# Kernel optimization log

Measured on AMD Instinct MI355X. Metric: run time of the kernel, lower is better.

## Reference

```python
import jax, jax.numpy as jnp
import numpy as np
import math

B, T, D, H, L, V = 2, 1024, 768, 12, 4, 50257
HD = D // H
ROPE_PCT = 0.5
MAX_WL = 10000.0
EPS = 1e-5


def setup_inputs() -> dict:
    key = jax.random.key(0)
    ks = jax.random.split(key, 8)
    s = 0.02
    return {
        "idx": jax.random.randint(ks[0], (B, T), 0, V, dtype=jnp.int32),
        "wte": jax.random.normal(ks[1], (V, D), jnp.float32) * s,
        "ln1_g": jnp.ones((L, D), jnp.float32),
        "ln1_b": jnp.zeros((L, D), jnp.float32),
        "Wqkv": jax.random.normal(ks[2], (L, D, 3 * D), jnp.float32) * s,
        "bqkv": jnp.zeros((L, 3 * D), jnp.float32),
        "Wo": jax.random.normal(ks[3], (L, D, D), jnp.float32) * s,
        "bo": jnp.zeros((L, D), jnp.float32),
        "ln2_g": jnp.ones((L, D), jnp.float32),
        "ln2_b": jnp.zeros((L, D), jnp.float32),
        "Wfc": jax.random.normal(ks[4], (L, D, 4 * D), jnp.float32) * s,
        "bfc": jnp.zeros((L, 4 * D), jnp.float32),
        "Wp": jax.random.normal(ks[5], (L, 4 * D, D), jnp.float32) * s,
        "bp": jnp.zeros((L, D), jnp.float32),
        "lnf_g": jnp.ones((D,), jnp.float32),
        "lnf_b": jnp.zeros((D,), jnp.float32),
        "Wlm": jax.random.normal(ks[6], (D, V), jnp.float32) * s,
    }


def _ln(x, g, b):
    m = x.mean(-1, keepdims=True)
    v = x.var(-1, keepdims=True)
    return (x - m) / jnp.sqrt(v + EPS) * g + b


def _gelu(x):
    return 0.5 * x * (1.0 + jnp.tanh(math.sqrt(2.0 / math.pi) * (x + 0.044715 * x ** 3)))


def _p_rope(x, positions):
    # x: [B, H, T, HD]; partial RoPE: rotate first ROPE_PCT of angle pairs, leave rest.
    rope_angles = int(ROPE_PCT * HD // 2)
    nope_angles = HD // 2 - rope_angles
    fraction = 2.0 * jnp.arange(0, rope_angles) / HD
    timescale = jnp.power(MAX_WL, fraction)
    timescale = jnp.pad(timescale, (0, nope_angles), constant_values=jnp.inf)
    sinusoid = positions[:, None] / timescale[None, :]  # [T, HD//2]; pos/inf = 0 -> no rotation
    sin, cos = jnp.sin(sinusoid), jnp.cos(sinusoid)
    first, second = jnp.split(x, 2, axis=-1)
    out = jnp.concatenate([first * cos - second * sin, second * cos + first * sin], axis=-1)
    return out.astype(x.dtype)


def reference(idx, wte, ln1_g, ln1_b, Wqkv, bqkv, Wo, bo, ln2_g, ln2_b, Wfc, bfc, Wp, bp, lnf_g, lnf_b, Wlm):
    x = wte[idx]  # [B, T, D]
    positions = jnp.arange(T, dtype=x.dtype)
    causal = jnp.tril(jnp.ones((T, T), dtype=bool))
    scale = jnp.sqrt(jnp.float32(HD)).astype(x.dtype)
    for l in range(L):
        h1 = _ln(x, ln1_g[l], ln1_b[l])
        h2 = _ln(x, ln2_g[l], ln2_b[l])  # note: both LNs read the same x (as in source)
        # attention
        qkv = h1 @ Wqkv[l] + bqkv[l]
        q, k, v = jnp.split(qkv, 3, axis=-1)
        sh = lambda t: t.reshape(B, T, H, HD).transpose(0, 2, 1, 3)
        q, k, v = sh(q), sh(k), sh(v)
        q = _p_rope(q, positions)
        k = _p_rope(k, positions)
        att = jnp.einsum('bhqd,bhkd->bhqk', q, k) / scale
        att = jnp.where(causal, att, jnp.finfo(att.dtype).min)
        att = jax.nn.softmax(att, axis=-1)
        y = jnp.einsum('bhqk,bhkd->bhqd', att, v)
        y = y.transpose(0, 2, 1, 3).reshape(B, T, D)
        x = x + (y @ Wo[l] + bo[l])
        # MLP
        h = _gelu(h2 @ Wfc[l] + bfc[l])
        x = x + (h @ Wp[l] + bp[l])
    x = _ln(x, lnf_g, lnf_b)
    logits = x @ Wlm  # [B, T, V]
    return logits
```

## Files before the change

kernel.cpp:

```cpp
#include <hip/hip_runtime.h>

typedef unsigned short u16;
typedef unsigned int u32;
typedef __attribute__((ext_vector_type(8))) short bf16x8;
typedef __attribute__((ext_vector_type(4))) float f32x4;

#define SEQ 1024
#define DM 768
#define NH 12
#define HD2 64
#define NLAYER 4
#define NVOCAB 50257
#define BT 2048

__device__ __forceinline__ u16 f2bf(float f) {
  union { float f; u32 u; } v; v.f = f;
  u32 r = v.u + 0x7FFFu + ((v.u >> 16) & 1u);
  return (u16)(r >> 16);
}
__device__ __forceinline__ float bf2f(u16 u) {
  union { u32 u; float f; } v; v.u = ((u32)u) << 16;
  return v.f;
}

__device__ __forceinline__ void glds16(const u16* g, u16* l) {
  __builtin_amdgcn_global_load_lds(
      (const __attribute__((address_space(1))) u32*)(const void*)g,
      (__attribute__((address_space(3))) u32*)(void*)l, 16, 0, 0);
}

__global__ void k_embed(const int* __restrict__ idx, const float* __restrict__ wte,
                        float* __restrict__ xf) {
  int r = blockIdx.x;
  int tok = idx[r];
  const float* s = wte + (size_t)tok * DM;
  float* d = xf + (size_t)r * DM;
  for (int c = threadIdx.x; c < DM; c += 256) d[c] = s[c];
}

__global__ void k_cvtT(const float* __restrict__ in, u16* __restrict__ out,
                       int R, int C) {
  __shared__ u16 t[32][34];
  int c0 = blockIdx.x * 32, r0 = blockIdx.y * 32;
  int tx = threadIdx.x & 31, ty = threadIdx.x >> 5;
#pragma unroll
  for (int i = 0; i < 4; ++i) {
    int r = r0 + ty + i * 8, c = c0 + tx;
    float v = (c < C) ? in[(size_t)r * C + c] : 0.f;
    t[ty + i * 8][tx] = f2bf(v);
  }
  __syncthreads();
  int cy = threadIdx.x >> 4;
  int rx = (threadIdx.x & 15) * 2;
#pragma unroll
  for (int i = 0; i < 2; ++i) {
    int c = c0 + cy + i * 16;
    if (c < C) {
      u32 wv = (u32)t[rx][cy + i * 16] | ((u32)t[rx + 1][cy + i * 16] << 16);
      *(u32*)&out[(size_t)c * R + r0 + rx] = wv;
    }
  }
}

__device__ __forceinline__ float bsum(float v, float* red) {
#pragma unroll
  for (int o = 32; o > 0; o >>= 1) v += __shfl_down(v, o);
  if ((threadIdx.x & 63) == 0) red[threadIdx.x >> 6] = v;
  __syncthreads();
  if (threadIdx.x == 0) red[4] = red[0] + red[1] + red[2] + red[3];
  __syncthreads();
  return red[4];
}

__global__ void k_ln(const float* __restrict__ x, const float* __restrict__ g1,
                     const float* __restrict__ b1, const float* __restrict__ g2,
                     const float* __restrict__ b2, u16* __restrict__ o1,
                     u16* __restrict__ o2) {
  __shared__ float red[8];
  int r = blockIdx.x;
  int t = threadIdx.x;
  const float* xr = x + (size_t)r * DM;
  float v0 = xr[t], v1 = xr[t + 256], v2 = xr[t + 512];
  float mean = bsum(v0 + v1 + v2, red) * (1.f / DM);
  float d0 = v0 - mean, d1 = v1 - mean, d2 = v2 - mean;
  float var = bsum(d0 * d0 + d1 * d1 + d2 * d2, red) * (1.f / DM);
  float rstd = rsqrtf(var + 1e-5f);
  u16* p1 = o1 + (size_t)r * DM;
  p1[t]       = f2bf(d0 * rstd * g1[t]       + b1[t]);
  p1[t + 256] = f2bf(d1 * rstd * g1[t + 256] + b1[t + 256]);
  p1[t + 512] = f2bf(d2 * rstd * g1[t + 512] + b1[t + 512]);
  if (o2) {
    u16* p2 = o2 + (size_t)r * DM;
    p2[t]       = f2bf(d0 * rstd * g2[t]       + b2[t]);
    p2[t + 256] = f2bf(d1 * rstd * g2[t + 256] + b2[t + 256]);
    p2[t + 512] = f2bf(d2 * rstd * g2[t + 512] + b2[t + 512]);
  }
}

__global__ void k_rope(const u16* __restrict__ qkvb, u16* __restrict__ qr,
                       u16* __restrict__ kr) {
  int gid = blockIdx.x * 256 + threadIdx.x;
  int j = gid & 31;
  int h = (gid >> 5) % NH;
  int t = (gid / (32 * NH)) & (SEQ - 1);
  int b = gid / (32 * NH * SEQ);
  float c = 1.f, s = 0.f;
  if (j < 16) {
    float inv = powf(10000.f, -(float)j * (1.f / 32.f));
    float ang = (float)t * inv;
    c = cosf(ang);
    s = sinf(ang);
  }
  size_t base = (size_t)(b * SEQ + t) * (3 * DM);
  size_t ob = ((size_t)(b * NH + h) * SEQ + t) * HD2 + j;
  {
    float a0 = bf2f(qkvb[base + h * HD2 + j]);
    float a1 = bf2f(qkvb[base + h * HD2 + j + 32]);
    qr[ob] = f2bf(a0 * c - a1 * s);
    qr[ob + 32] = f2bf(a1 * c + a0 * s);
  }
  {
    float a0 = bf2f(qkvb[base + DM + h * HD2 + j]);
    float a1 = bf2f(qkvb[base + DM + h * HD2 + j + 32]);
    kr[ob] = f2bf(a0 * c - a1 * s);
    kr[ob + 32] = f2bf(a1 * c + a0 * s);
  }
}

__global__ void k_vtrans(const u16* __restrict__ qkvb, u16* __restrict__ vT) {
  __shared__ u16 tile[64][65];
  int t0 = blockIdx.x * 64;
  int bh = blockIdx.y;
  int b = bh / NH, h = bh % NH;
  int rr = threadIdx.x >> 2, seg = threadIdx.x & 3;
  const u16* src = qkvb + (size_t)(b * SEQ + t0 + rr) * (3 * DM) + 2 * DM + h * HD2;
#pragma unroll
  for (int i = 0; i < 16; ++i) tile[rr][seg * 16 + i] = src[seg * 16 + i];
  __syncthreads();
  u16* dst = vT + ((size_t)bh * HD2 + rr) * SEQ + t0;
#pragma unroll
  for (int i = 0; i < 16; ++i) dst[seg * 16 + i] = tile[seg * 16 + i][rr];
}

__global__ void k_attn(const u16* __restrict__ qr, const u16* __restrict__ kr,
                       const u16* __restrict__ vT, u16* __restrict__ yb) {
  int ti = (int)gridDim.x - 1 - (int)blockIdx.x;
  int bh = blockIdx.y;
  __shared__ u16 Ps[64 * 72];
  __shared__ u16 Ks[2][4096];
  __shared__ u16 Vs[2][4096];
  int tid = threadIdx.x;
  int rr = tid >> 2, cc = tid & 3;
  int w = tid >> 6, l = tid & 63;
  int rl = l & 15, g = l >> 4;
  {
    const u16* gq = qr + ((size_t)bh * SEQ + ti * 64 + rr) * HD2;
    *(uint4*)&Ps[rr * 72 + cc * 8]      = *(const uint4*)(gq + cc * 8);
    *(uint4*)&Ps[rr * 72 + cc * 8 + 32] = *(const uint4*)(gq + cc * 8 + 32);
  }
  int srow = w * 8 + (l >> 3);
  int gs = (l & 7) ^ (l >> 3);
  const u16* gkb = kr + (size_t)bh * SEQ * HD2;
  const u16* gvb = vT + (size_t)bh * HD2 * SEQ;
  glds16(gkb + (size_t)(0 * 64 + srow) * 64 + gs * 8,      &Ks[0][w * 512]);
  glds16(gkb + (size_t)(0 * 64 + 32 + srow) * 64 + gs * 8, &Ks[0][2048 + w * 512]);
  glds16(gvb + (size_t)srow * SEQ + 0 * 64 + gs * 8,       &Vs[0][w * 512]);
  glds16(gvb + (size_t)(32 + srow) * SEQ + 0 * 64 + gs * 8,&Vs[0][2048 + w * 512]);
  __syncthreads();
  bf16x8 aq0 = *(const bf16x8*)&Ps[(w * 16 + rl) * 72 + g * 8];
  bf16x8 aq1 = *(const bf16x8*)&Ps[(w * 16 + rl) * 72 + 32 + g * 8];
  float m[4], lsum[4];
  f32x4 oacc[4] = {};
#pragma unroll
  for (int r2 = 0; r2 < 4; ++r2) { m[r2] = -3.0e38f; lsum[r2] = 0.f; }
  int qloc = w * 16 + g * 4;
  int sw = rl & 7;
  int cur = 0;
  for (int kt = 0; kt <= ti; ++kt) {
    if (kt < ti) {
      int nx = cur ^ 1;
      glds16(gkb + (size_t)((kt + 1) * 64 + srow) * 64 + gs * 8,      &Ks[nx][w * 512]);
      glds16(gkb + (size_t)((kt + 1) * 64 + 32 + srow) * 64 + gs * 8, &Ks[nx][2048 + w * 512]);
      glds16(gvb + (size_t)srow * SEQ + (kt + 1) * 64 + gs * 8,       &Vs[nx][w * 512]);
      glds16(gvb + (size_t)(32 + srow) * SEQ + (kt + 1) * 64 + gs * 8,&Vs[nx][2048 + w * 512]);
    }
    f32x4 s[4] = {};
    __builtin_amdgcn_s_setprio(1);
#pragma unroll
    for (int nt = 0; nt < 4; ++nt) {
      int r = (nt * 16 + rl) * 64;
      bf16x8 b0 = *(const bf16x8*)&Ks[cur][r + ((0 + g) ^ sw) * 8];
      bf16x8 b1 = *(const bf16x8*)&Ks[cur][r + ((4 + g) ^ sw) * 8];
      s[nt] = __builtin_amdgcn_mfma_f32_16x16x32_bf16(aq0, b0, s[nt], 0, 0, 0);
      s[nt] = __builtin_amdgcn_mfma_f32_16x16x32_bf16(aq1, b1, s[nt], 0, 0, 0);
    }
    __builtin_amdgcn_s_setprio(0);
#pragma unroll
    for (int nt = 0; nt < 4; ++nt) s[nt] *= 0.125f;
    if (kt == ti) {
#pragma unroll
      for (int nt = 0; nt < 4; ++nt) {
        int col = nt * 16 + rl;
#pragma unroll
        for (int r2 = 0; r2 < 4; ++r2)
          if (col > qloc + r2) s[nt][r2] = -3.0e38f;
      }
    }
#pragma unroll
    for (int r2 = 0; r2 < 4; ++r2) {
      float pm = fmaxf(fmaxf(s[0][r2], s[1][r2]), fmaxf(s[2][r2], s[3][r2]));
#pragma unroll
      for (int o = 1; o < 16; o <<= 1) pm = fmaxf(pm, __shfl_xor(pm, o));
      float mn = fmaxf(m[r2], pm);
      float corr = __expf(m[r2] - mn);
      float p0 = __expf(s[0][r2] - mn);
      float p1 = __expf(s[1][r2] - mn);
      float p2 = __expf(s[2][r2] - mn);
      float p3 = __expf(s[3][r2] - mn);
      float ps = p0 + p1 + p2 + p3;
#pragma unroll
      for (int o = 1; o < 16; o <<= 1) ps += __shfl_xor(ps, o);
      lsum[r2] = lsum[r2] * corr + ps;
      m[r2] = mn;
      oacc[0][r2] *= corr; oacc[1][r2] *= corr;
      oacc[2][r2] *= corr; oacc[3][r2] *= corr;
      int prow = (qloc + r2) * 72;
      Ps[prow + rl]      = f2bf(p0);
      Ps[prow + 16 + rl] = f2bf(p1);
      Ps[prow + 32 + rl] = f2bf(p2);
      Ps[prow + 48 + rl] = f2bf(p3);
    }
    bf16x8 pa0 = *(const bf16x8*)&Ps[(w * 16 + rl) * 72 + g * 8];
    bf16x8 pa1 = *(const bf16x8*)&Ps[(w * 16 + rl) * 72 + 32 + g * 8];
    __builtin_amdgcn_s_setprio(1);
#pragma unroll
    for (int nt = 0; nt < 4; ++nt) {
      int r = (nt * 16 + rl) * 64;
      bf16x8 b0 = *(const bf16x8*)&Vs[cur][r + ((0 + g) ^ sw) * 8];
      bf16x8 b1 = *(const bf16x8*)&Vs[cur][r + ((4 + g) ^ sw) * 8];
      oacc[nt] = __builtin_amdgcn_mfma_f32_16x16x32_bf16(pa0, b0, oacc[nt], 0, 0, 0);
      oacc[nt] = __builtin_amdgcn_mfma_f32_16x16x32_bf16(pa1, b1, oacc[nt], 0, 0, 0);
    }
    __builtin_amdgcn_s_setprio(0);
    __syncthreads();
    cur ^= 1;
  }
  int b = bh / NH, h = bh % NH;
  float invl[4];
#pragma unroll
  for (int r2 = 0; r2 < 4; ++r2) invl[r2] = 1.f / lsum[r2];
#pragma unroll
  for (int nt = 0; nt < 4; ++nt) {
    int d = nt * 16 + rl;
#pragma unroll
    for (int r2 = 0; r2 < 4; ++r2) {
      int trow = ti * 64 + qloc + r2;
      yb[((size_t)(b * SEQ + trow)) * DM + h * HD2 + d] = f2bf(oacc[nt][r2] * invl[r2]);
    }
  }
}

__global__ void k_logits(const u16* __restrict__ A, const u16* __restrict__ Bt,
                         float* __restrict__ outf, int M, int N, int K, int MT) {
  __shared__ u16 SM[16384];
  float* cw = (float*)SM;
  int nwg = gridDim.x;
  int id = blockIdx.x;
  if ((nwg & 7) == 0) id = (id & 7) * (nwg >> 3) + (id >> 3);
  int mt = id % MT, nt = id / MT;
  int m0 = mt * 128, n0 = nt * 128;
  int tid = threadIdx.x;
  int w = tid >> 6, l = tid & 63;
  int srow = w * 16 + (l >> 2);
  int gs = (l & 3) ^ ((l >> 3) & 3);
  const u16* gA0 = A + (size_t)(m0 + srow) * K + gs * 8;
  const u16* gA1 = A + (size_t)(m0 + 64 + srow) * K + gs * 8;
  int rb0 = n0 + srow;      if (rb0 > N - 1) rb0 = N - 1;
  int rb1 = n0 + 64 + srow; if (rb1 > N - 1) rb1 = N - 1;
  const u16* gB0 = Bt + (size_t)rb0 * K + gs * 8;
  const u16* gB1 = Bt + (size_t)rb1 * K + gs * 8;
  int wm = (w >> 1) * 64, wn = (w & 1) * 64;
  int rl = l & 15, g = l >> 4;
  int sla = g ^ ((rl >> 1) & 3);
  f32x4 acc[4][4] = {};
  int nK = K >> 5;
  int cur = 0;
  {
    u16* dA = SM + w * 512;
    glds16(gA0, dA); glds16(gA1, dA + 2048);
    u16* dB = SM + 4096 + w * 512;
    glds16(gB0, dB); glds16(gB1, dB + 2048);
  }
  __syncthreads();
  for (int kt = 0; kt < nK; ++kt) {
    if (kt + 1 < nK) {
      u16* dA = SM + (cur ^ 1) * 8192 + w * 512;
      glds16(gA0 + (kt + 1) * 32, dA); glds16(gA1 + (kt + 1) * 32, dA + 2048);
      u16* dB = dA + 4096;
      glds16(gB0 + (kt + 1) * 32, dB); glds16(gB1 + (kt + 1) * 32, dB + 2048);
    }
    const u16* As = SM + cur * 8192;
    const u16* Bs = As + 4096;
    bf16x8 af[4], bfr[4];
    __builtin_amdgcn_s_setprio(1);
#pragma unroll
    for (int i = 0; i < 4; ++i)
      af[i] = *(const bf16x8*)&As[(wm + i * 16 + rl) * 32 + sla * 8];
#pragma unroll
    for (int j = 0; j < 4; ++j)
      bfr[j] = *(const bf16x8*)&Bs[(wn + j * 16 + rl) * 32 + sla * 8];
#pragma unroll
    for (int i = 0; i < 4; ++i)
#pragma unroll
      for (int j = 0; j < 4; ++j)
        acc[i][j] = __builtin_amdgcn_mfma_f32_16x16x32_bf16(af[i], bfr[j],
                                                            acc[i][j], 0, 0, 0);
    __builtin_amdgcn_s_setprio(0);
    __syncthreads();
    cur ^= 1;
  }
  for (int ch = 0; ch < 4; ++ch) {
    if ((w >> 1) == (ch >> 1)) {
      int ib = (ch & 1) * 2;
#pragma unroll
      for (int ii = 0; ii < 2; ++ii) {
#pragma unroll
        for (int j = 0; j < 4; ++j) {
          int col = wn + j * 16 + rl;
#pragma unroll
          for (int r2 = 0; r2 < 4; ++r2) {
            int rowc = ii * 16 + g * 4 + r2;
            cw[rowc * 132 + col] = acc[ib + ii][j][r2];
          }
        }
      }
    }
    __syncthreads();
    for (int t = tid; t < 4096; t += 256) {
      int rowc = t >> 7, col = t & 127;
      int gc = n0 + col;
      if (gc < N)
        __builtin_nontemporal_store(cw[rowc * 132 + col],
                                    &outf[(size_t)(m0 + ch * 32 + rowc) * N + gc]);
    }
    __syncthreads();
  }
}

__global__ void k_gemm64(const u16* __restrict__ A, const u16* __restrict__ Bt,
                         const float* __restrict__ bias, u16* __restrict__ outb,
                         float* __restrict__ outf, int M, int N, int K, int MT,
                         int mode) {
  __shared__ u16 As[8192];
  __shared__ u16 Bs[8192];
  int nwg = gridDim.x;
  int id = blockIdx.x;
  if ((nwg & 7) == 0) id = (id & 7) * (nwg >> 3) + (id >> 3);
  int mt = id % MT, nt = id / MT;
  int sk = blockIdx.y, nsk = gridDim.y;
  int Kc = K / nsk, k0 = sk * Kc;
  int m0 = mt * 64, n0 = nt * 64;
  int tid = threadIdx.x;
  int w = tid >> 6, l = tid & 63;
  int row0 = tid >> 3, slot0 = tid & 7;
  int gs0 = slot0 ^ (row0 & 7);
  const u16* gA0 = A + (size_t)(m0 + row0) * K + k0 + gs0 * 8;
  const u16* gA1 = gA0 + (size_t)32 * K;
  const u16* gB0 = Bt + (size_t)(n0 + row0) * K + k0 + gs0 * 8;
  const u16* gB1 = gB0 + (size_t)32 * K;
  int wm = (w >> 1) * 32, wn = (w & 1) * 32;
  int rl = l & 15, g = l >> 4;
  int sl0 = g ^ (rl & 7), sl1 = (4 + g) ^ (rl & 7);
  f32x4 acc[2][2] = {};
  int nK = Kc >> 6;
  int cur = 0;
  {
    glds16(gA0, As + w * 512); glds16(gA1, As + 2048 + w * 512);
    glds16(gB0, Bs + w * 512); glds16(gB1, Bs + 2048 + w * 512);
  }
  __syncthreads();
  for (int kt = 0; kt < nK; ++kt) {
    if (kt + 1 < nK) {
      int nx = (cur ^ 1) * 4096;
      glds16(gA0 + (kt + 1) * 64, As + nx + w * 512);
      glds16(gA1 + (kt + 1) * 64, As + nx + 2048 + w * 512);
      glds16(gB0 + (kt + 1) * 64, Bs + nx + w * 512);
      glds16(gB1 + (kt + 1) * 64, Bs + nx + 2048 + w * 512);
    }
    const u16* Ac = As + cur * 4096;
    const u16* Bc = Bs + cur * 4096;
    bf16x8 a0[2], a1[2], b0[2], b1[2];
    __builtin_amdgcn_s_setprio(1);
#pragma unroll
    for (int i = 0; i < 2; ++i) {
      int r = (wm + i * 16 + rl) * 64;
      a0[i] = *(const bf16x8*)&Ac[r + sl0 * 8];
      a1[i] = *(const bf16x8*)&Ac[r + sl1 * 8];
    }
#pragma unroll
    for (int j = 0; j < 2; ++j) {
      int r = (wn + j * 16 + rl) * 64;
      b0[j] = *(const bf16x8*)&Bc[r + sl0 * 8];
      b1[j] = *(const bf16x8*)&Bc[r + sl1 * 8];
    }
#pragma unroll
    for (int i = 0; i < 2; ++i)
#pragma unroll
      for (int j = 0; j < 2; ++j) {
        acc[i][j] = __builtin_amdgcn_mfma_f32_16x16x32_bf16(a0[i], b0[j],
                                                            acc[i][j], 0, 0, 0);
        acc[i][j] = __builtin_amdgcn_mfma_f32_16x16x32_bf16(a1[i], b1[j],
                                                            acc[i][j], 0, 0, 0);
      }
    __builtin_amdgcn_s_setprio(0);
    __syncthreads();
    cur ^= 1;
  }
#pragma unroll
  for (int i = 0; i < 2; ++i) {
#pragma unroll
    for (int j = 0; j < 2; ++j) {
      int col = n0 + wn + j * 16 + rl;
      float bv = bias ? bias[col] : 0.f;
#pragma unroll
      for (int r2 = 0; r2 < 4; ++r2) {
        int row = m0 + wm + i * 16 + g * 4 + r2;
        size_t oi = (size_t)row * N + col;
        float v = acc[i][j][r2];
        if (mode == 0) {
          outb[oi] = f2bf(v + bv);
        } else if (mode == 1) {
          v += bv;
          float u = 0.7978845608028654f * (v + 0.044715f * v * v * v);
          outb[oi] = f2bf(0.5f * v * (1.f + tanhf(u)));
        } else {
          if (sk == 0) v += bv;
          atomicAdd(&outf[oi], v);
        }
      }
    }
  }
}

__global__ void k_gemm_f32b(const u16* __restrict__ A, const float* __restrict__ B,
                            float* __restrict__ outf, int M, int N, int K) {
  __shared__ u16 As[128 * 40];
  __shared__ u16 Bs[4 * 128 * 12];
  int tid = threadIdx.x;
  int wid = tid >> 6, lane = tid & 63;
  int rl = lane & 15, g = lane >> 4;
  int m0 = blockIdx.x * 128, n0 = blockIdx.y * 128;
  int wm = (wid >> 1) * 64, wn = (wid & 1) * 64;
  int ar = tid >> 2, ac = tid & 3;
  int bn = tid & 127, bq = tid >> 7;
  f32x4 acc[4][4] = {};
  int nK = K / 32;
  for (int kt = 0; kt < nK; ++kt) {
    __syncthreads();
    {
      const u16* ga = A + (size_t)(m0 + ar) * K + kt * 32 + ac * 8;
      *(uint4*)&As[ar * 40 + ac * 8] = *(const uint4*)ga;
      *(uint4*)&As[(ar + 64) * 40 + ac * 8] = *(const uint4*)(ga + (size_t)64 * K);
    }
    int col = n0 + bn;
#pragma unroll
    for (int r = 0; r < 4; ++r) {
      int kq = bq + 2 * r;
      int kk = kt * 32 + kq * 4;
      float f0 = 0.f, f1 = 0.f, f2v = 0.f, f3 = 0.f;
      if (col < N) {
        const float* gb = B + (size_t)kk * N + col;
        f0 = gb[0]; f1 = gb[(size_t)N]; f2v = gb[(size_t)2 * N]; f3 = gb[(size_t)3 * N];
      }
      uint2 wv;
      wv.x = (u32)f2bf(f0) | ((u32)f2bf(f1) << 16);
      wv.y = (u32)f2bf(f2v) | ((u32)f2bf(f3) << 16);
      *(uint2*)&Bs[(kq >> 1) * 1536 + bn * 12 + (kq & 1) * 4] = wv;
    }
    __syncthreads();
    bf16x8 af[4], bfr[4];
#pragma unroll
    for (int mt = 0; mt < 4; ++mt)
      af[mt] = *(const bf16x8*)&As[(wm + mt * 16 + rl) * 40 + g * 8];
#pragma unroll
    for (int nt = 0; nt < 4; ++nt) {
      const u16* p = &Bs[g * 1536 + (wn + nt * 16 + rl) * 12];
      union { bf16x8 v; uint2 u2[2]; } tmp;
      tmp.u2[0] = *(const uint2*)p;
      tmp.u2[1] = *(const uint2*)(p + 4);
      bfr[nt] = tmp.v;
    }
#pragma unroll
    for (int mt = 0; mt < 4; ++mt)
#pragma unroll
      for (int nt = 0; nt < 4; ++nt)
        acc[mt][nt] = __builtin_amdgcn_mfma_f32_16x16x32_bf16(af[mt], bfr[nt],
                                                              acc[mt][nt], 0, 0, 0);
  }
#pragma unroll
  for (int mt = 0; mt < 4; ++mt)
#pragma unroll
    for (int nt = 0; nt < 4; ++nt) {
      int col = n0 + wn + nt * 16 + rl;
      if (col >= N) continue;
#pragma unroll
      for (int r2 = 0; r2 < 4; ++r2) {
        int row = m0 + wm + mt * 16 + g * 4 + r2;
        outf[(size_t)row * N + col] = acc[mt][nt][r2];
      }
    }
}

extern "C" void kernel_launch(void* const* d_in, const int* in_sizes, int n_in,
                              void* d_out, int out_size, void* d_ws, size_t ws_size,
                              hipStream_t stream) {
  (void)in_sizes; (void)n_in; (void)out_size;
  const int*   idx  = (const int*)  d_in[0];
  const float* wte  = (const float*)d_in[1];
  const float* ln1g = (const float*)d_in[2];
  const float* ln1b = (const float*)d_in[3];
  const float* Wqkv = (const float*)d_in[4];
  const float* bqkv = (const float*)d_in[5];
  const float* Wo   = (const float*)d_in[6];
  const float* bo   = (const float*)d_in[7];
  const float* ln2g = (const float*)d_in[8];
  const float* ln2b = (const float*)d_in[9];
  const float* Wfc  = (const float*)d_in[10];
  const float* bfc  = (const float*)d_in[11];
  const float* Wp   = (const float*)d_in[12];
  const float* bp   = (const float*)d_in[13];
  const float* lnfg = (const float*)d_in[14];
  const float* lnfb = (const float*)d_in[15];
  const float* Wlm  = (const float*)d_in[16];
  float* out = (float*)d_out;

  char* sb = (char*)d_out;
  size_t off = 0;
  auto alloc = [&](size_t bytes) {
    char* p = sb + off;
    off += (bytes + 255) & ~(size_t)255;
    return (void*)p;
  };
  float* xf  = (float*)alloc((size_t)BT * DM * 4);
  u16* h1b   = (u16*)alloc((size_t)BT * DM * 2);
  u16* h2b   = (u16*)alloc((size_t)BT * DM * 2);
  u16* qkvb  = (u16*)alloc((size_t)BT * 3 * DM * 2);
  u16* qr    = (u16*)alloc((size_t)BT * DM * 2);
  u16* kr    = (u16*)alloc((size_t)BT * DM * 2);
  u16* vT    = (u16*)alloc((size_t)BT * DM * 2);
  u16* yb    = (u16*)alloc((size_t)BT * DM * 2);
  u16* hgel  = (u16*)alloc((size_t)BT * 4 * DM * 2);
  u16* wqkvT = (u16*)alloc((size_t)NLAYER * 3 * DM * DM * 2);
  u16* woT   = (u16*)alloc((size_t)NLAYER * DM * DM * 2);
  u16* wfcT  = (u16*)alloc((size_t)NLAYER * 4 * DM * DM * 2);
  u16* wpT   = (u16*)alloc((size_t)NLAYER * 4 * DM * DM * 2);

  size_t wlmT_bytes = (size_t)NVOCAB * DM * 2;
  size_t xlnf_bytes = (size_t)BT * DM * 2;
  bool fast_lm = ws_size >= wlmT_bytes + xlnf_bytes + 512;
  u16* wlmT = (u16*)d_ws;
  u16* xlnf = fast_lm ? (u16*)((char*)d_ws + ((wlmT_bytes + 255) & ~(size_t)255))
                      : (u16*)d_ws;

  for (int l = 0; l < NLAYER; ++l) {
    k_cvtT<<<dim3((3 * DM + 31) / 32, DM / 32), 256, 0, stream>>>(
        Wqkv + (size_t)l * DM * 3 * DM, wqkvT + (size_t)l * 3 * DM * DM, DM, 3 * DM);
    k_cvtT<<<dim3(DM / 32, DM / 32), 256, 0, stream>>>(
        Wo + (size_t)l * DM * DM, woT + (size_t)l * DM * DM, DM, DM);
    k_cvtT<<<dim3((4 * DM) / 32, DM / 32), 256, 0, stream>>>(
        Wfc + (size_t)l * DM * 4 * DM, wfcT + (size_t)l * 4 * DM * DM, DM, 4 * DM);
    k_cvtT<<<dim3(DM / 32, (4 * DM) / 32), 256, 0, stream>>>(
        Wp + (size_t)l * 4 * DM * DM, wpT + (size_t)l * 4 * DM * DM, 4 * DM, DM);
  }
  if (fast_lm)
    k_cvtT<<<dim3((NVOCAB + 31) / 32, DM / 32), 256, 0, stream>>>(Wlm, wlmT, DM, NVOCAB);

  k_embed<<<BT, 256, 0, stream>>>(idx, wte, xf);
  for (int l = 0; l < NLAYER; ++l) {
    k_ln<<<BT, 256, 0, stream>>>(xf, ln1g + l * DM, ln1b + l * DM,
                                 ln2g + l * DM, ln2b + l * DM, h1b, h2b);
    k_gemm64<<<dim3((BT / 64) * (3 * DM / 64), 1), 256, 0, stream>>>(
        h1b, wqkvT + (size_t)l * 3 * DM * DM, bqkv + (size_t)l * 3 * DM,
        qkvb, nullptr, BT, 3 * DM, DM, BT / 64, 0);
    k_rope<<<(2 * SEQ * NH * 32) / 256, 256, 0, stream>>>(qkvb, qr, kr);
    k_vtrans<<<dim3(SEQ / 64, 2 * NH), 256, 0, stream>>>(qkvb, vT);
    k_attn<<<dim3(SEQ / 64, 2 * NH), 256, 0, stream>>>(qr, kr, vT, yb);
    k_gemm64<<<dim3((BT / 64) * (DM / 64), 2), 256, 0, stream>>>(
        yb, woT + (size_t)l * DM * DM, bo + (size_t)l * DM,
        nullptr, xf, BT, DM, DM, BT / 64, 2);
    k_gemm64<<<dim3((BT / 64) * (4 * DM / 64), 1), 256, 0, stream>>>(
        h2b, wfcT + (size_t)l * 4 * DM * DM, bfc + (size_t)l * 4 * DM,
        hgel, nullptr, BT, 4 * DM, DM, BT / 64, 1);
    k_gemm64<<<dim3((BT / 64) * (DM / 64), 4), 256, 0, stream>>>(
        hgel, wpT + (size_t)l * 4 * DM * DM, bp + (size_t)l * DM,
        nullptr, xf, BT, DM, 4 * DM, BT / 64, 2);
  }
  k_ln<<<BT, 256, 0, stream>>>(xf, lnfg, lnfb, nullptr, nullptr, xlnf, nullptr);
  if (fast_lm) {
    int nt = (NVOCAB + 127) / 128;
    k_logits<<<(BT / 128) * nt, 256, 0, stream>>>(
        xlnf, wlmT, out, BT, NVOCAB, DM, BT / 128);
  } else {
    k_gemm_f32b<<<dim3(BT / 128, (NVOCAB + 127) / 128), 256, 0, stream>>>(
        xlnf, Wlm, out, BT, NVOCAB, DM);
  }
}
```

Baseline: 1.037 ms.

## Generalize 128-tile GEMM for QKV/FC, vectorize weight transpose, relax barriers

Turns the logits GEMM into a general 128x128-tile kernel with bias, GELU and bf16 output modes, and routes the QKV and FC projections to it instead of the 64-tile GEMM. The weight convert-transpose kernel now uses 64x64 tiles with float4 loads. Both GEMM main loops replace __syncthreads with explicit vmcnt waits plus s_barrier so prefetch loads can stay in flight across the barrier. The aim is more data reuse per tile, fewer weight-prep transactions and fewer load stalls, at the cost of fewer workgroups for the mid-size GEMMs and fragile hand-written wait counts.

```diff
diff --git a/kernel.cpp b/kernel.cpp
--- a/kernel.cpp
+++ b/kernel.cpp
@@ -40,24 +40,36 @@
 
 __global__ void k_cvtT(const float* __restrict__ in, u16* __restrict__ out,
                        int R, int C) {
-  __shared__ u16 t[32][34];
-  int c0 = blockIdx.x * 32, r0 = blockIdx.y * 32;
-  int tx = threadIdx.x & 31, ty = threadIdx.x >> 5;
+  __shared__ u16 t[64][68];
+  int c0 = blockIdx.x * 64, r0 = blockIdx.y * 64;
+  int tx = threadIdx.x & 15, ty = threadIdx.x >> 4;
+  int c = c0 + tx * 4;
 #pragma unroll
   for (int i = 0; i < 4; ++i) {
-    int r = r0 + ty + i * 8, c = c0 + tx;
-    float v = (c < C) ? in[(size_t)r * C + c] : 0.f;
-    t[ty + i * 8][tx] = f2bf(v);
+    int r = r0 + ty + i * 16;
+    float4 v = make_float4(0.f, 0.f, 0.f, 0.f);
+    if (c + 3 < C) {
+      v = *(const float4*)&in[(size_t)r * C + c];
+    } else {
+      if (c + 0 < C) v.x = in[(size_t)r * C + c];
+      if (c + 1 < C) v.y = in[(size_t)r * C + c + 1];
+      if (c + 2 < C) v.z = in[(size_t)r * C + c + 2];
+      if (c + 3 < C) v.w = in[(size_t)r * C + c + 3];
+    }
+    t[ty + i * 16][tx * 4 + 0] = f2bf(v.x);
+    t[ty + i * 16][tx * 4 + 1] = f2bf(v.y);
+    t[ty + i * 16][tx * 4 + 2] = f2bf(v.z);
+    t[ty + i * 16][tx * 4 + 3] = f2bf(v.w);
   }
   __syncthreads();
-  int cy = threadIdx.x >> 4;
-  int rx = (threadIdx.x & 15) * 2;
-#pragma unroll
-  for (int i = 0; i < 2; ++i) {
-    int c = c0 + cy + i * 16;
-    if (c < C) {
-      u32 wv = (u32)t[rx][cy + i * 16] | ((u32)t[rx + 1][cy + i * 16] << 16);
-      *(u32*)&out[(size_t)c * R + r0 + rx] = wv;
+  int wl = threadIdx.x & 31, grp = threadIdx.x >> 5;
+#pragma unroll
+  for (int it = 0; it < 8; ++it) {
+    int cc = it * 8 + grp;
+    int gcol = c0 + cc;
+    if (gcol < C) {
+      u32 wv = (u32)t[2 * wl][cc] | ((u32)t[2 * wl + 1][cc] << 16);
+      *(u32*)&out[(size_t)gcol * R + r0 + 2 * wl] = wv;
     }
   }
 }
@@ -162,10 +174,10 @@
   int gs = (l & 7) ^ (l >> 3);
   const u16* gkb = kr + (size_t)bh * SEQ * HD2;
   const u16* gvb = vT + (size_t)bh * HD2 * SEQ;
-  glds16(gkb + (size_t)(0 * 64 + srow) * 64 + gs * 8,      &Ks[0][w * 512]);
-  glds16(gkb + (size_t)(0 * 64 + 32 + srow) * 64 + gs * 8, &Ks[0][2048 + w * 512]);
-  glds16(gvb + (size_t)srow * SEQ + 0 * 64 + gs * 8,       &Vs[0][w * 512]);
-  glds16(gvb + (size_t)(32 + srow) * SEQ + 0 * 64 + gs * 8,&Vs[0][2048 + w * 512]);
+  glds16(gkb + (size_t)srow * 64 + gs * 8,        &Ks[0][w * 512]);
+  glds16(gkb + (size_t)(32 + srow) * 64 + gs * 8, &Ks[0][2048 + w * 512]);
+  glds16(gvb + (size_t)srow * SEQ + gs * 8,       &Vs[0][w * 512]);
+  glds16(gvb + (size_t)(32 + srow) * SEQ + gs * 8,&Vs[0][2048 + w * 512]);
   __syncthreads();
   bf16x8 aq0 = *(const bf16x8*)&Ps[(w * 16 + rl) * 72 + g * 8];
   bf16x8 aq1 = *(const bf16x8*)&Ps[(w * 16 + rl) * 72 + 32 + g * 8];
@@ -260,8 +272,10 @@
   }
 }
 
-__global__ void k_logits(const u16* __restrict__ A, const u16* __restrict__ Bt,
-                         float* __restrict__ outf, int M, int N, int K, int MT) {
+__global__ void k_gemm128(const u16* __restrict__ A, const u16* __restrict__ Bt,
+                          const float* __restrict__ bias, u16* __restrict__ outb,
+                          float* __restrict__ outf, int M, int N, int K, int MT,
+                          int mode) {
   __shared__ u16 SM[16384];
   float* cw = (float*)SM;
   int nwg = gridDim.x;
@@ -299,6 +313,11 @@
       u16* dB = dA + 4096;
       glds16(gB0 + (kt + 1) * 32, dB); glds16(gB1 + (kt + 1) * 32, dB + 2048);
     }
+    __builtin_amdgcn_sched_barrier(0);
+    if (kt + 1 < nK) asm volatile("s_waitcnt vmcnt(4)" ::: "memory");
+    else             asm volatile("s_waitcnt vmcnt(0)" ::: "memory");
+    __builtin_amdgcn_s_barrier();
+    __builtin_amdgcn_sched_barrier(0);
     const u16* As = SM + cur * 8192;
     const u16* Bs = As + 4096;
     bf16x8 af[4], bfr[4];
@@ -316,7 +335,9 @@
         acc[i][j] = __builtin_amdgcn_mfma_f32_16x16x32_bf16(af[i], bfr[j],
                                                             acc[i][j], 0, 0, 0);
     __builtin_amdgcn_s_setprio(0);
-    __syncthreads();
+    __builtin_amdgcn_sched_barrier(0);
+    __builtin_amdgcn_s_barrier();
+    __builtin_amdgcn_sched_barrier(0);
     cur ^= 1;
   }
   for (int ch = 0; ch < 4; ++ch) {
@@ -330,18 +351,35 @@
 #pragma unroll
           for (int r2 = 0; r2 < 4; ++r2) {
             int rowc = ii * 16 + g * 4 + r2;
-            cw[rowc * 132 + col] = acc[ib + ii][j][r2];
+            float v = acc[ib + ii][j][r2];
+            if (mode != 3) {
+              v += bias[n0 + col];
+              if (mode == 1) {
+                float u = 0.7978845608028654f * (v + 0.044715f * v * v * v);
+                v = 0.5f * v * (1.f + tanhf(u));
+              }
+            }
+            cw[rowc * 132 + col] = v;
           }
         }
       }
     }
     __syncthreads();
-    for (int t = tid; t < 4096; t += 256) {
-      int rowc = t >> 7, col = t & 127;
-      int gc = n0 + col;
-      if (gc < N)
-        __builtin_nontemporal_store(cw[rowc * 132 + col],
-                                    &outf[(size_t)(m0 + ch * 32 + rowc) * N + gc]);
+    if (mode == 3) {
+      for (int t = tid; t < 4096; t += 256) {
+        int rowc = t >> 7, col = t & 127;
+        int gc = n0 + col;
+        if (gc < N)
+          __builtin_nontemporal_store(cw[rowc * 132 + col],
+                                      &outf[(size_t)(m0 + ch * 32 + rowc) * N + gc]);
+      }
+    } else {
+      for (int t = tid; t < 2048; t += 256) {
+        int rowc = t >> 6, cp = t & 63;
+        u32 wv = (u32)f2bf(cw[rowc * 132 + 2 * cp]) |
+                 ((u32)f2bf(cw[rowc * 132 + 2 * cp + 1]) << 16);
+        *(u32*)&outb[(size_t)(m0 + ch * 32 + rowc) * N + n0 + 2 * cp] = wv;
+      }
     }
     __syncthreads();
   }
@@ -387,6 +425,11 @@
       glds16(gB0 + (kt + 1) * 64, Bs + nx + w * 512);
       glds16(gB1 + (kt + 1) * 64, Bs + nx + 2048 + w * 512);
     }
+    __builtin_amdgcn_sched_barrier(0);
+    if (kt + 1 < nK) asm volatile("s_waitcnt vmcnt(4)" ::: "memory");
+    else             asm volatile("s_waitcnt vmcnt(0)" ::: "memory");
+    __builtin_amdgcn_s_barrier();
+    __builtin_amdgcn_sched_barrier(0);
     const u16* Ac = As + cur * 4096;
     const u16* Bc = Bs + cur * 4096;
     bf16x8 a0[2], a1[2], b0[2], b1[2];
@@ -413,7 +456,9 @@
                                                             acc[i][j], 0, 0, 0);
       }
     __builtin_amdgcn_s_setprio(0);
-    __syncthreads();
+    __builtin_amdgcn_sched_barrier(0);
+    __builtin_amdgcn_s_barrier();
+    __builtin_amdgcn_sched_barrier(0);
     cur ^= 1;
   }
 #pragma unroll
@@ -563,34 +608,34 @@
                       : (u16*)d_ws;
 
   for (int l = 0; l < NLAYER; ++l) {
-    k_cvtT<<<dim3((3 * DM + 31) / 32, DM / 32), 256, 0, stream>>>(
+    k_cvtT<<<dim3((3 * DM + 63) / 64, DM / 64), 256, 0, stream>>>(
         Wqkv + (size_t)l * DM * 3 * DM, wqkvT + (size_t)l * 3 * DM * DM, DM, 3 * DM);
-    k_cvtT<<<dim3(DM / 32, DM / 32), 256, 0, stream>>>(
+    k_cvtT<<<dim3(DM / 64, DM / 64), 256, 0, stream>>>(
         Wo + (size_t)l * DM * DM, woT + (size_t)l * DM * DM, DM, DM);
-    k_cvtT<<<dim3((4 * DM) / 32, DM / 32), 256, 0, stream>>>(
+    k_cvtT<<<dim3((4 * DM) / 64, DM / 64), 256, 0, stream>>>(
         Wfc + (size_t)l * DM * 4 * DM, wfcT + (size_t)l * 4 * DM * DM, DM, 4 * DM);
-    k_cvtT<<<dim3(DM / 32, (4 * DM) / 32), 256, 0, stream>>>(
+    k_cvtT<<<dim3(DM / 64, (4 * DM) / 64), 256, 0, stream>>>(
         Wp + (size_t)l * 4 * DM * DM, wpT + (size_t)l * 4 * DM * DM, 4 * DM, DM);
   }
   if (fast_lm)
-    k_cvtT<<<dim3((NVOCAB + 31) / 32, DM / 32), 256, 0, stream>>>(Wlm, wlmT, DM, NVOCAB);
+    k_cvtT<<<dim3((NVOCAB + 63) / 64, DM / 64), 256, 0, stream>>>(Wlm, wlmT, DM, NVOCAB);
 
   k_embed<<<BT, 256, 0, stream>>>(idx, wte, xf);
   for (int l = 0; l < NLAYER; ++l) {
     k_ln<<<BT, 256, 0, stream>>>(xf, ln1g + l * DM, ln1b + l * DM,
                                  ln2g + l * DM, ln2b + l * DM, h1b, h2b);
-    k_gemm64<<<dim3((BT / 64) * (3 * DM / 64), 1), 256, 0, stream>>>(
+    k_gemm128<<<(BT / 128) * (3 * DM / 128), 256, 0, stream>>>(
         h1b, wqkvT + (size_t)l * 3 * DM * DM, bqkv + (size_t)l * 3 * DM,
-        qkvb, nullptr, BT, 3 * DM, DM, BT / 64, 0);
+        qkvb, nullptr, BT, 3 * DM, DM, BT / 128, 0);
     k_rope<<<(2 * SEQ * NH * 32) / 256, 256, 0, stream>>>(qkvb, qr, kr);
     k_vtrans<<<dim3(SEQ / 64, 2 * NH), 256, 0, stream>>>(qkvb, vT);
     k_attn<<<dim3(SEQ / 64, 2 * NH), 256, 0, stream>>>(qr, kr, vT, yb);
     k_gemm64<<<dim3((BT / 64) * (DM / 64), 2), 256, 0, stream>>>(
         yb, woT + (size_t)l * DM * DM, bo + (size_t)l * DM,
         nullptr, xf, BT, DM, DM, BT / 64, 2);
-    k_gemm64<<<dim3((BT / 64) * (4 * DM / 64), 1), 256, 0, stream>>>(
+    k_gemm128<<<(BT / 128) * (4 * DM / 128), 256, 0, stream>>>(
         h2b, wfcT + (size_t)l * 4 * DM * DM, bfc + (size_t)l * 4 * DM,
-        hgel, nullptr, BT, 4 * DM, DM, BT / 64, 1);
+        hgel, nullptr, BT, 4 * DM, DM, BT / 128, 1);
     k_gemm64<<<dim3((BT / 64) * (DM / 64), 4), 256, 0, stream>>>(
         hgel, wpT + (size_t)l * 4 * DM * DM, bp + (size_t)l * DM,
         nullptr, xf, BT, DM, 4 * DM, BT / 64, 2);
@@ -598,8 +643,8 @@
   k_ln<<<BT, 256, 0, stream>>>(xf, lnfg, lnfb, nullptr, nullptr, xlnf, nullptr);
   if (fast_lm) {
     int nt = (NVOCAB + 127) / 128;
-    k_logits<<<(BT / 128) * nt, 256, 0, stream>>>(
-        xlnf, wlmT, out, BT, NVOCAB, DM, BT / 128);
+    k_gemm128<<<(BT / 128) * nt, 256, 0, stream>>>(
+        xlnf, wlmT, nullptr, nullptr, out, BT, NVOCAB, DM, BT / 128, 3);
   } else {
     k_gemm_f32b<<<dim3(BT / 128, (NVOCAB + 127) / 128), 256, 0, stream>>>(
         xlnf, Wlm, out, BT, NVOCAB, DM);
```

Measured after the change: 1.573 ms. 51.6% more time.
